# Kernel optimization log

Measured on AMD Instinct MI355X. Metric: run time of the kernel, lower is better.

The kernel has to match this reference:

```python
import jax, jax.numpy as jnp
import numpy as np

H = 32          # phasor harmonics
DELTA0 = 7.0    # base phasor frequency
HID = 128       # hidden_dim
NEXP = 4        # num_experts
EDIM = 64       # expert_dim
NCLS = 3        # num_classes
IN_DIM = 28 * 28
ENH_DIM = HID + 2 * H  # 192


def setup_inputs() -> dict:
    key = jax.random.key(0)
    ks = jax.random.split(key, 12)
    B = 65536
    s = lambda d: 1.0 / np.sqrt(d)
    return {
        "x": jax.random.normal(ks[0], (B, 28, 28), dtype=jnp.float32),
        "W_in": jax.random.normal(ks[1], (IN_DIM, HID), dtype=jnp.float32) * s(IN_DIM),
        "b_in": jnp.zeros((HID,), dtype=jnp.float32),
        "W_gate": jax.random.normal(ks[2], (ENH_DIM, NEXP), dtype=jnp.float32) * s(ENH_DIM),
        "b_gate": jnp.zeros((NEXP,), dtype=jnp.float32),
        "W_exp": jax.random.normal(ks[3], (NEXP, ENH_DIM, EDIM), dtype=jnp.float32) * s(ENH_DIM),
        "b_exp": jnp.zeros((NEXP, EDIM), dtype=jnp.float32),
        "W_ctx": jax.random.normal(ks[4], (EDIM, HID), dtype=jnp.float32) * s(EDIM),
        "b_ctx": jnp.zeros((HID,), dtype=jnp.float32),
        "W_out": jax.random.normal(ks[5], (HID, NCLS), dtype=jnp.float32) * s(HID),
        "b_out": jnp.zeros((NCLS,), dtype=jnp.float32),
    }


def _phasor_bank(t):
    # t: [B] scalar drive per sample -> [B, 2H] cos/sin harmonic features
    freqs = DELTA0 * jnp.arange(1, H + 1, dtype=t.dtype)  # [H]
    phase = t[:, None] * freqs[None, :]                   # [B, H]
    return jnp.concatenate([jnp.cos(phase), jnp.sin(phase)], axis=-1)


def reference(x, W_in, b_in, W_gate, b_gate, W_exp, b_exp, W_ctx, b_ctx, W_out, b_out):
    B = x.shape[0]
    x_flat = x.reshape((B, -1))                                  # [B, 784]
    projected = x_flat @ W_in + b_in                             # [B, HID]
    t = jnp.mean(projected, axis=-1)                             # [B]
    temporal = _phasor_bank(t)                                   # [B, 2H]
    enhanced = jnp.concatenate([projected, temporal], axis=-1)   # [B, ENH_DIM]
    # Expert retrieval core: softmax gate over NEXP experts
    gate = jax.nn.softmax(enhanced @ W_gate + b_gate, axis=-1)   # [B, NEXP]
    expert_out = jax.nn.relu(
        jnp.einsum('bd,edh->beh', enhanced, W_exp) + b_exp[None] # [B, NEXP, EDIM]
    )
    combined = jnp.einsum('be,beh->bh', gate, expert_out)        # [B, EDIM]
    context = jnp.tanh(combined @ W_ctx + b_ctx)                 # [B, HID]
    logits = context @ W_out + b_out                             # [B, NCLS]
    return logits
```

## Files before the change

### kernel.cpp

```cpp
#include <hip/hip_runtime.h>

typedef unsigned short u16;
typedef unsigned int u32;
typedef __attribute__((ext_vector_type(8))) short short8;
typedef __attribute__((ext_vector_type(4))) float f32x4;

#define OFF_WM    0
#define OFF_WINF  3584
#define OFF_WEGF  208384
#define OFF_WCTXF 312832
#define OFF_WOUTF 329216

__device__ __forceinline__ u16 f2bf(float x) {
  union { float f; u32 u; } v; v.f = x;
  u32 r = v.u + 0x7FFFu + ((v.u >> 16) & 1u);
  return (u16)(r >> 16);
}

__global__ void prep_kernel(const float* __restrict__ W_in, const float* __restrict__ b_in,
                            const float* __restrict__ W_gate, const float* __restrict__ W_exp,
                            const float* __restrict__ W_ctx, const float* __restrict__ W_out,
                            float* __restrict__ wm, u16* __restrict__ WinF,
                            u16* __restrict__ WegF, u16* __restrict__ WctxF,
                            u16* __restrict__ WoutF) {
  int idx = blockIdx.x * 256 + threadIdx.x;
  if (idx < 801) {
    if (idx == 800) {
      float s = 0.f;
      for (int j = 0; j < 128; ++j) s += b_in[j];
      wm[800] = s * (1.f / 128.f);
    } else if (idx >= 784) {
      wm[idx] = 0.f;
    } else {
      float s = 0.f;
      for (int j = 0; j < 128; ++j) s += W_in[idx * 128 + j];
      wm[idx] = s * (1.f / 128.f);
    }
  } else if (idx < 103201) {
    int f = idx - 801;
    int j = f & 7, lane = (f >> 3) & 63, tile = f >> 9;
    int ct = tile & 7, kt = tile >> 3;
    int k = kt * 32 + ((lane >> 4) << 3) + j;
    int n = ct * 16 + (lane & 15);
    WinF[f] = (k < 784) ? f2bf(W_in[k * 128 + n]) : (u16)0;
  } else if (idx < 155425) {
    int f = idx - 103201;
    int j = f & 7, lane = (f >> 3) & 63, tile = f >> 9;
    int kt = tile / 17, ct = tile - kt * 17;
    int k = kt * 32 + ((lane >> 4) << 3) + j;
    int n = ct * 16 + (lane & 15);
    float v = 0.f;
    if (n < 256) { int e = n >> 6, h = n & 63; v = W_exp[(e * 192 + k) * 64 + h]; }
    else if (n < 260) v = W_gate[k * 4 + (n - 256)];
    WegF[f] = f2bf(v);
  } else if (idx < 163617) {
    int f = idx - 155425;
    int j = f & 7, lane = (f >> 3) & 63, tile = f >> 9;
    int ct = tile & 7, kt = tile >> 3;
    int k = kt * 32 + ((lane >> 4) << 3) + j;
    int n = ct * 16 + (lane & 15);
    WctxF[f] = f2bf(W_ctx[k * 128 + n]);
  } else if (idx < 165665) {
    int f = idx - 163617;
    int j = f & 7, lane = (f >> 3) & 63, kt = f >> 9;
    int k = kt * 32 + ((lane >> 4) << 3) + j;
    int n = lane & 15;
    WoutF[f] = (n < 3) ? f2bf(W_out[k * 3 + n]) : (u16)0;
  }
}

__global__ __launch_bounds__(256, 4)
void fused_kernel(const float* __restrict__ x,
                  const float* __restrict__ b_in, const float* __restrict__ b_gate,
                  const float* __restrict__ b_exp, const float* __restrict__ b_ctx,
                  const float* __restrict__ b_out,
                  const float* __restrict__ wm, const u16* __restrict__ WinF,
                  const u16* __restrict__ WegF, const u16* __restrict__ WctxF,
                  const u16* __restrict__ WoutF,
                  float* __restrict__ out) {
  __shared__ __align__(16) u16 smem[4 * 3840];
  const int tid = threadIdx.x;
  const int wv = tid >> 6;
  const int ln = tid & 63;
  const int cb = ln & 15;
  const int qr = ln >> 4;
  u16* enhW = smem + wv * 3840;
  u16* cmbW = enhW;
  u16* ctxW = enhW + 1280;

  const int grow = blockIdx.x * 64 + wv * 16;
  const float* xr = x + (size_t)(grow + cb) * 784;

  const f32x4 vz = {0.f, 0.f, 0.f, 0.f};

  f32x4 acc[8];
  #pragma unroll
  for (int i = 0; i < 8; ++i) acc[i] = vz;
  float tp = 0.f;

  for (int kt = 0; kt < 25; ++kt) {
    const int k0 = kt * 32 + qr * 8;
    float4 a0 = make_float4(0.f, 0.f, 0.f, 0.f);
    float4 a1 = make_float4(0.f, 0.f, 0.f, 0.f);
    if (k0 < 784) {
      a0 = *(const float4*)(xr + k0);
      a1 = *(const float4*)(xr + k0 + 4);
      const float4 m0 = *(const float4*)(wm + k0);
      const float4 m1 = *(const float4*)(wm + k0 + 4);
      tp += a0.x * m0.x + a0.y * m0.y + a0.z * m0.z + a0.w * m0.w
          + a1.x * m1.x + a1.y * m1.y + a1.z * m1.z + a1.w * m1.w;
    }
    union { short8 s; u32 u[4]; } af;
    af.u[0] = (u32)f2bf(a0.x) | ((u32)f2bf(a0.y) << 16);
    af.u[1] = (u32)f2bf(a0.z) | ((u32)f2bf(a0.w) << 16);
    af.u[2] = (u32)f2bf(a1.x) | ((u32)f2bf(a1.y) << 16);
    af.u[3] = (u32)f2bf(a1.z) | ((u32)f2bf(a1.w) << 16);
    const u16* wb = WinF + (size_t)kt * 8 * 512 + ln * 8;
    #pragma unroll
    for (int ct = 0; ct < 8; ++ct) {
      short8 Bf = *(const short8*)(wb + ct * 512);
      acc[ct] = __builtin_amdgcn_mfma_f32_16x16x32_bf16(af.s, Bf, acc[ct], 0, 0, 0);
    }
  }

  tp += __shfl_xor(tp, 16);
  tp += __shfl_xor(tp, 32);
  const float t = tp + wm[800];

  #pragma unroll
  for (int ct = 0; ct < 8; ++ct) {
    float bi = b_in[ct * 16 + cb];
    u16* dst = enhW + (ct >> 1) * 640 + (ct & 1) * 16 + cb;
    #pragma unroll
    for (int i = 0; i < 4; ++i)
      dst[(qr * 4 + i) * 40] = f2bf(acc[ct][i] + bi);
  }
  {
    float phi = 7.f * t;
    float ss, cc, sd, cd;
    sincosf(phi * (float)(qr * 8 + 1), &ss, &cc);
    sincosf(phi, &sd, &cd);
    u16* pc = enhW + 4 * 640 + cb * 40 + qr * 8;
    u16* ps = enhW + 5 * 640 + cb * 40 + qr * 8;
    #pragma unroll
    for (int m = 0; m < 8; ++m) {
      pc[m] = f2bf(cc);
      ps[m] = f2bf(ss);
      float nc = cc * cd - ss * sd;
      ss = ss * cd + cc * sd;
      cc = nc;
    }
  }

  f32x4 accg = vz;
  #pragma unroll
  for (int kt = 0; kt < 6; ++kt) {
    short8 Af = *(const short8*)(enhW + kt * 640 + cb * 40 + qr * 8);
    short8 Bf = *(const short8*)(WegF + ((kt * 17 + 16) * 64 + ln) * 8);
    accg = __builtin_amdgcn_mfma_f32_16x16x32_bf16(Af, Bf, accg, 0, 0, 0);
  }
  float ge[4][4];
  {
    float bg = b_gate[cb & 3];
    #pragma unroll
    for (int i = 0; i < 4; ++i) {
      float gi = accg[i] + bg;
      float mx = fmaxf(gi, __shfl_xor(gi, 1));
      mx = fmaxf(mx, __shfl_xor(mx, 2));
      float ev = __expf(gi - mx);
      float sv = ev + __shfl_xor(ev, 1);
      sv += __shfl_xor(sv, 2);
      float g = ev / sv;
      int base = qr * 16;
      ge[0][i] = __shfl(g, base + 0);
      ge[1][i] = __shfl(g, base + 1);
      ge[2][i] = __shfl(g, base + 2);
      ge[3][i] = __shfl(g, base + 3);
    }
  }
  f32x4 cmb[4];
  #pragma unroll
  for (int i = 0; i < 4; ++i) cmb[i] = vz;
  #pragma unroll
  for (int e = 0; e < 4; ++e) {
    f32x4 ae[4];
    #pragma unroll
    for (int i = 0; i < 4; ++i) ae[i] = vz;
    #pragma unroll
    for (int kt = 0; kt < 6; ++kt) {
      short8 Af = *(const short8*)(enhW + kt * 640 + cb * 40 + qr * 8);
      #pragma unroll
      for (int c2 = 0; c2 < 4; ++c2) {
        short8 Bf = *(const short8*)(WegF + ((kt * 17 + e * 4 + c2) * 64 + ln) * 8);
        ae[c2] = __builtin_amdgcn_mfma_f32_16x16x32_bf16(Af, Bf, ae[c2], 0, 0, 0);
      }
    }
    #pragma unroll
    for (int c2 = 0; c2 < 4; ++c2) {
      float be = b_exp[e * 64 + c2 * 16 + cb];
      #pragma unroll
      for (int i = 0; i < 4; ++i)
        cmb[c2][i] += ge[e][i] * fmaxf(ae[c2][i] + be, 0.f);
    }
  }
  #pragma unroll
  for (int c2 = 0; c2 < 4; ++c2) {
    u16* dst = cmbW + (c2 >> 1) * 640 + (c2 & 1) * 16 + cb;
    #pragma unroll
    for (int i = 0; i < 4; ++i)
      dst[(qr * 4 + i) * 40] = f2bf(cmb[c2][i]);
  }

  f32x4 acc3[8];
  #pragma unroll
  for (int i = 0; i < 8; ++i) acc3[i] = vz;
  #pragma unroll
  for (int kt = 0; kt < 2; ++kt) {
    short8 Af = *(const short8*)(cmbW + kt * 640 + cb * 40 + qr * 8);
    #pragma unroll
    for (int ct = 0; ct < 8; ++ct) {
      short8 Bf = *(const short8*)(WctxF + ((kt * 8 + ct) * 64 + ln) * 8);
      acc3[ct] = __builtin_amdgcn_mfma_f32_16x16x32_bf16(Af, Bf, acc3[ct], 0, 0, 0);
    }
  }
  #pragma unroll
  for (int ct = 0; ct < 8; ++ct) {
    float bc = b_ctx[ct * 16 + cb];
    u16* dst = ctxW + ct * 16 + cb;
    #pragma unroll
    for (int i = 0; i < 4; ++i) {
      float v = acc3[ct][i] + bc;
      float ex = __expf(2.f * v);
      dst[(qr * 4 + i) * 136] = f2bf(1.f - 2.f / (ex + 1.f));
    }
  }

  f32x4 acc4 = vz;
  #pragma unroll
  for (int kt = 0; kt < 4; ++kt) {
    short8 Af = *(const short8*)(ctxW + cb * 136 + kt * 32 + qr * 8);
    short8 Bf = *(const short8*)(WoutF + (kt * 64 + ln) * 8);
    acc4 = __builtin_amdgcn_mfma_f32_16x16x32_bf16(Af, Bf, acc4, 0, 0, 0);
  }
  if (cb < 3) {
    float bo = b_out[cb];
    #pragma unroll
    for (int i = 0; i < 4; ++i)
      out[(size_t)(grow + qr * 4 + i) * 3 + cb] = acc4[i] + bo;
  }
}

extern "C" void kernel_launch(void* const* d_in, const int* in_sizes, int n_in,
                              void* d_out, int out_size, void* d_ws, size_t ws_size,
                              hipStream_t stream) {
  const float* x      = (const float*)d_in[0];
  const float* W_in   = (const float*)d_in[1];
  const float* b_in   = (const float*)d_in[2];
  const float* W_gate = (const float*)d_in[3];
  const float* b_gate = (const float*)d_in[4];
  const float* W_exp  = (const float*)d_in[5];
  const float* b_exp  = (const float*)d_in[6];
  const float* W_ctx  = (const float*)d_in[7];
  const float* b_ctx  = (const float*)d_in[8];
  const float* W_out  = (const float*)d_in[9];
  const float* b_out  = (const float*)d_in[10];
  float* out = (float*)d_out;

  char* ws = (char*)d_ws;
  float* wm  = (float*)(ws + OFF_WM);
  u16* WinF  = (u16*)(ws + OFF_WINF);
  u16* WegF  = (u16*)(ws + OFF_WEGF);
  u16* WctxF = (u16*)(ws + OFF_WCTXF);
  u16* WoutF = (u16*)(ws + OFF_WOUTF);

  const int B = in_sizes[0] / 784;
  prep_kernel<<<648, 256, 0, stream>>>(W_in, b_in, W_gate, W_exp, W_ctx, W_out,
                                       wm, WinF, WegF, WctxF, WoutF);
  fused_kernel<<<B / 64, 256, 0, stream>>>(x, b_in, b_gate, b_exp, b_ctx, b_out,
                                           wm, WinF, WegF, WctxF, WoutF, out);
}
```

Measured before the change: 342.8 us.

## Process two 16-row tiles per wave to reuse weight fragments

Each wave now handles 32 rows (two 16-row MFMA tiles) instead of 16, so every B-fragment weight load from global memory is shared by two MFMAs throughout all stages. The weight fragments for the input projection are preloaded per k-step before the activation loads. The grid is halved, LDS per block doubles, and launch bounds drop to 2 blocks per SM, trading occupancy and register pressure for fewer weight reads per row.

```diff
diff --git a/kernel.cpp b/kernel.cpp
--- a/kernel.cpp
+++ b/kernel.cpp
@@ -69,7 +69,7 @@
   }
 }
 
-__global__ __launch_bounds__(256, 4)
+__global__ __launch_bounds__(256, 2)
 void fused_kernel(const float* __restrict__ x,
                   const float* __restrict__ b_in, const float* __restrict__ b_gate,
                   const float* __restrict__ b_exp, const float* __restrict__ b_ctx,
@@ -78,70 +78,99 @@
                   const u16* __restrict__ WegF, const u16* __restrict__ WctxF,
                   const u16* __restrict__ WoutF,
                   float* __restrict__ out) {
-  __shared__ __align__(16) u16 smem[4 * 3840];
+  __shared__ __align__(16) u16 smem[4 * 7680];
   const int tid = threadIdx.x;
   const int wv = tid >> 6;
   const int ln = tid & 63;
   const int cb = ln & 15;
   const int qr = ln >> 4;
-  u16* enhW = smem + wv * 3840;
-  u16* cmbW = enhW;
-  u16* ctxW = enhW + 1280;
-
-  const int grow = blockIdx.x * 64 + wv * 16;
-  const float* xr = x + (size_t)(grow + cb) * 784;
+  u16* enh0 = smem + wv * 7680;
+  u16* enh1 = enh0 + 3840;
+  u16* cmb0 = enh0;
+  u16* cmb1 = enh1;
+  u16* ctx0 = enh0 + 1280;
+  u16* ctx1 = enh1 + 1280;
+
+  const int grow = blockIdx.x * 128 + wv * 32;
+  const float* xr0 = x + (size_t)(grow + cb) * 784;
+  const float* xr1 = xr0 + (size_t)16 * 784;
 
   const f32x4 vz = {0.f, 0.f, 0.f, 0.f};
 
-  f32x4 acc[8];
-  #pragma unroll
-  for (int i = 0; i < 8; ++i) acc[i] = vz;
-  float tp = 0.f;
-
+  f32x4 acc0[8], acc1[8];
+  #pragma unroll
+  for (int i = 0; i < 8; ++i) { acc0[i] = vz; acc1[i] = vz; }
+  float tp0 = 0.f, tp1 = 0.f;
+
+  const u16* wbase = WinF + ln * 8;
   for (int kt = 0; kt < 25; ++kt) {
+    const u16* wb = wbase + (size_t)kt * 4096;
+    short8 Bf[8];
+    #pragma unroll
+    for (int ct = 0; ct < 8; ++ct)
+      Bf[ct] = *(const short8*)(wb + ct * 512);
+
     const int k0 = kt * 32 + qr * 8;
-    float4 a0 = make_float4(0.f, 0.f, 0.f, 0.f);
-    float4 a1 = make_float4(0.f, 0.f, 0.f, 0.f);
+    float4 a0 = make_float4(0.f, 0.f, 0.f, 0.f), a1 = a0;
+    float4 b0 = a0, b1 = a0, m0 = a0, m1 = a0;
     if (k0 < 784) {
-      a0 = *(const float4*)(xr + k0);
-      a1 = *(const float4*)(xr + k0 + 4);
-      const float4 m0 = *(const float4*)(wm + k0);
-      const float4 m1 = *(const float4*)(wm + k0 + 4);
-      tp += a0.x * m0.x + a0.y * m0.y + a0.z * m0.z + a0.w * m0.w
-          + a1.x * m1.x + a1.y * m1.y + a1.z * m1.z + a1.w * m1.w;
-    }
-    union { short8 s; u32 u[4]; } af;
+      a0 = *(const float4*)(xr0 + k0);
+      a1 = *(const float4*)(xr0 + k0 + 4);
+      b0 = *(const float4*)(xr1 + k0);
+      b1 = *(const float4*)(xr1 + k0 + 4);
+      m0 = *(const float4*)(wm + k0);
+      m1 = *(const float4*)(wm + k0 + 4);
+      tp0 += a0.x * m0.x + a0.y * m0.y + a0.z * m0.z + a0.w * m0.w
+           + a1.x * m1.x + a1.y * m1.y + a1.z * m1.z + a1.w * m1.w;
+      tp1 += b0.x * m0.x + b0.y * m0.y + b0.z * m0.z + b0.w * m0.w
+           + b1.x * m1.x + b1.y * m1.y + b1.z * m1.z + b1.w * m1.w;
+    }
+    union { short8 s; u32 u[4]; } af, bf;
     af.u[0] = (u32)f2bf(a0.x) | ((u32)f2bf(a0.y) << 16);
     af.u[1] = (u32)f2bf(a0.z) | ((u32)f2bf(a0.w) << 16);
     af.u[2] = (u32)f2bf(a1.x) | ((u32)f2bf(a1.y) << 16);
     af.u[3] = (u32)f2bf(a1.z) | ((u32)f2bf(a1.w) << 16);
-    const u16* wb = WinF + (size_t)kt * 8 * 512 + ln * 8;
+    bf.u[0] = (u32)f2bf(b0.x) | ((u32)f2bf(b0.y) << 16);
+    bf.u[1] = (u32)f2bf(b0.z) | ((u32)f2bf(b0.w) << 16);
+    bf.u[2] = (u32)f2bf(b1.x) | ((u32)f2bf(b1.y) << 16);
+    bf.u[3] = (u32)f2bf(b1.z) | ((u32)f2bf(b1.w) << 16);
+
     #pragma unroll
     for (int ct = 0; ct < 8; ++ct) {
-      short8 Bf = *(const short8*)(wb + ct * 512);
-      acc[ct] = __builtin_amdgcn_mfma_f32_16x16x32_bf16(af.s, Bf, acc[ct], 0, 0, 0);
-    }
-  }
-
-  tp += __shfl_xor(tp, 16);
-  tp += __shfl_xor(tp, 32);
-  const float t = tp + wm[800];
+      acc0[ct] = __builtin_amdgcn_mfma_f32_16x16x32_bf16(af.s, Bf[ct], acc0[ct], 0, 0, 0);
+      acc1[ct] = __builtin_amdgcn_mfma_f32_16x16x32_bf16(bf.s, Bf[ct], acc1[ct], 0, 0, 0);
+    }
+  }
+
+  tp0 += __shfl_xor(tp0, 16);
+  tp0 += __shfl_xor(tp0, 32);
+  tp1 += __shfl_xor(tp1, 16);
+  tp1 += __shfl_xor(tp1, 32);
+  const float mb = wm[800];
+  const float t0 = tp0 + mb;
+  const float t1 = tp1 + mb;
 
   #pragma unroll
   for (int ct = 0; ct < 8; ++ct) {
     float bi = b_in[ct * 16 + cb];
-    u16* dst = enhW + (ct >> 1) * 640 + (ct & 1) * 16 + cb;
-    #pragma unroll
-    for (int i = 0; i < 4; ++i)
-      dst[(qr * 4 + i) * 40] = f2bf(acc[ct][i] + bi);
-  }
-  {
+    u16* d0 = enh0 + (ct >> 1) * 640 + (ct & 1) * 16 + cb;
+    u16* d1 = enh1 + (ct >> 1) * 640 + (ct & 1) * 16 + cb;
+    #pragma unroll
+    for (int i = 0; i < 4; ++i) {
+      d0[(qr * 4 + i) * 40] = f2bf(acc0[ct][i] + bi);
+      d1[(qr * 4 + i) * 40] = f2bf(acc1[ct][i] + bi);
+    }
+  }
+  #pragma unroll
+  for (int g = 0; g < 2; ++g) {
+    float t = g ? t1 : t0;
+    u16* eW = g ? enh1 : enh0;
     float phi = 7.f * t;
     float ss, cc, sd, cd;
     sincosf(phi * (float)(qr * 8 + 1), &ss, &cc);
     sincosf(phi, &sd, &cd);
-    u16* pc = enhW + 4 * 640 + cb * 40 + qr * 8;
-    u16* ps = enhW + 5 * 640 + cb * 40 + qr * 8;
+    u16* pc = eW + 4 * 640 + cb * 40 + qr * 8;
+    u16* ps = eW + 5 * 640 + cb * 40 + qr * 8;
     #pragma unroll
     for (int m = 0; m < 8; ++m) {
       pc[m] = f2bf(cc);
@@ -152,101 +181,140 @@
     }
   }
 
-  f32x4 accg = vz;
+  const u16* gbase = WegF + ln * 8;
+  f32x4 g0 = vz, g1 = vz;
   #pragma unroll
   for (int kt = 0; kt < 6; ++kt) {
-    short8 Af = *(const short8*)(enhW + kt * 640 + cb * 40 + qr * 8);
-    short8 Bf = *(const short8*)(WegF + ((kt * 17 + 16) * 64 + ln) * 8);
-    accg = __builtin_amdgcn_mfma_f32_16x16x32_bf16(Af, Bf, accg, 0, 0, 0);
-  }
-  float ge[4][4];
+    short8 A0 = *(const short8*)(enh0 + kt * 640 + cb * 40 + qr * 8);
+    short8 A1 = *(const short8*)(enh1 + kt * 640 + cb * 40 + qr * 8);
+    short8 Bg = *(const short8*)(gbase + (size_t)(kt * 17 + 16) * 512);
+    g0 = __builtin_amdgcn_mfma_f32_16x16x32_bf16(A0, Bg, g0, 0, 0, 0);
+    g1 = __builtin_amdgcn_mfma_f32_16x16x32_bf16(A1, Bg, g1, 0, 0, 0);
+  }
+
+  float ge0[4][4], ge1[4][4];
   {
     float bg = b_gate[cb & 3];
     #pragma unroll
     for (int i = 0; i < 4; ++i) {
-      float gi = accg[i] + bg;
-      float mx = fmaxf(gi, __shfl_xor(gi, 1));
-      mx = fmaxf(mx, __shfl_xor(mx, 2));
-      float ev = __expf(gi - mx);
-      float sv = ev + __shfl_xor(ev, 1);
-      sv += __shfl_xor(sv, 2);
-      float g = ev / sv;
-      int base = qr * 16;
-      ge[0][i] = __shfl(g, base + 0);
-      ge[1][i] = __shfl(g, base + 1);
-      ge[2][i] = __shfl(g, base + 2);
-      ge[3][i] = __shfl(g, base + 3);
-    }
-  }
-  f32x4 cmb[4];
-  #pragma unroll
-  for (int i = 0; i < 4; ++i) cmb[i] = vz;
+      {
+        float gi = g0[i] + bg;
+        float mx = fmaxf(gi, __shfl_xor(gi, 1));
+        mx = fmaxf(mx, __shfl_xor(mx, 2));
+        float ev = __expf(gi - mx);
+        float sv = ev + __shfl_xor(ev, 1);
+        sv += __shfl_xor(sv, 2);
+        float g = ev / sv;
+        int base = qr * 16;
+        ge0[0][i] = __shfl(g, base + 0);
+        ge0[1][i] = __shfl(g, base + 1);
+        ge0[2][i] = __shfl(g, base + 2);
+        ge0[3][i] = __shfl(g, base + 3);
+      }
+      {
+        float gi = g1[i] + bg;
+        float mx = fmaxf(gi, __shfl_xor(gi, 1));
+        mx = fmaxf(mx, __shfl_xor(mx, 2));
+        float ev = __expf(gi - mx);
+        float sv = ev + __shfl_xor(ev, 1);
+        sv += __shfl_xor(sv, 2);
+        float g = ev / sv;
+        int base = qr * 16;
+        ge1[0][i] = __shfl(g, base + 0);
+        ge1[1][i] = __shfl(g, base + 1);
+        ge1[2][i] = __shfl(g, base + 2);
+        ge1[3][i] = __shfl(g, base + 3);
+      }
+    }
+  }
+
+  f32x4 cA[4], cB[4];
+  #pragma unroll
+  for (int i = 0; i < 4; ++i) { cA[i] = vz; cB[i] = vz; }
   #pragma unroll
   for (int e = 0; e < 4; ++e) {
-    f32x4 ae[4];
-    #pragma unroll
-    for (int i = 0; i < 4; ++i) ae[i] = vz;
+    f32x4 ae0[4], ae1[4];
+    #pragma unroll
+    for (int i = 0; i < 4; ++i) { ae0[i] = vz; ae1[i] = vz; }
     #pragma unroll
     for (int kt = 0; kt < 6; ++kt) {
-      short8 Af = *(const short8*)(enhW + kt * 640 + cb * 40 + qr * 8);
+      short8 A0 = *(const short8*)(enh0 + kt * 640 + cb * 40 + qr * 8);
+      short8 A1 = *(const short8*)(enh1 + kt * 640 + cb * 40 + qr * 8);
+      const u16* gb = gbase + (size_t)(kt * 17 + e * 4) * 512;
       #pragma unroll
       for (int c2 = 0; c2 < 4; ++c2) {
-        short8 Bf = *(const short8*)(WegF + ((kt * 17 + e * 4 + c2) * 64 + ln) * 8);
-        ae[c2] = __builtin_amdgcn_mfma_f32_16x16x32_bf16(Af, Bf, ae[c2], 0, 0, 0);
+        short8 Bf = *(const short8*)(gb + c2 * 512);
+        ae0[c2] = __builtin_amdgcn_mfma_f32_16x16x32_bf16(A0, Bf, ae0[c2], 0, 0, 0);
+        ae1[c2] = __builtin_amdgcn_mfma_f32_16x16x32_bf16(A1, Bf, ae1[c2], 0, 0, 0);
       }
     }
     #pragma unroll
     for (int c2 = 0; c2 < 4; ++c2) {
       float be = b_exp[e * 64 + c2 * 16 + cb];
       #pragma unroll
-      for (int i = 0; i < 4; ++i)
-        cmb[c2][i] += ge[e][i] * fmaxf(ae[c2][i] + be, 0.f);
+      for (int i = 0; i < 4; ++i) {
+        cA[c2][i] += ge0[e][i] * fmaxf(ae0[c2][i] + be, 0.f);
+        cB[c2][i] += ge1[e][i] * fmaxf(ae1[c2][i] + be, 0.f);
+      }
     }
   }
   #pragma unroll
   for (int c2 = 0; c2 < 4; ++c2) {
-    u16* dst = cmbW + (c2 >> 1) * 640 + (c2 & 1) * 16 + cb;
-    #pragma unroll
-    for (int i = 0; i < 4; ++i)
-      dst[(qr * 4 + i) * 40] = f2bf(cmb[c2][i]);
-  }
-
-  f32x4 acc3[8];
-  #pragma unroll
-  for (int i = 0; i < 8; ++i) acc3[i] = vz;
+    u16* d0 = cmb0 + (c2 >> 1) * 640 + (c2 & 1) * 16 + cb;
+    u16* d1 = cmb1 + (c2 >> 1) * 640 + (c2 & 1) * 16 + cb;
+    #pragma unroll
+    for (int i = 0; i < 4; ++i) {
+      d0[(qr * 4 + i) * 40] = f2bf(cA[c2][i]);
+      d1[(qr * 4 + i) * 40] = f2bf(cB[c2][i]);
+    }
+  }
+
+  f32x4 c30[8], c31[8];
+  #pragma unroll
+  for (int i = 0; i < 8; ++i) { c30[i] = vz; c31[i] = vz; }
   #pragma unroll
   for (int kt = 0; kt < 2; ++kt) {
-    short8 Af = *(const short8*)(cmbW + kt * 640 + cb * 40 + qr * 8);
+    short8 A0 = *(const short8*)(cmb0 + kt * 640 + cb * 40 + qr * 8);
+    short8 A1 = *(const short8*)(cmb1 + kt * 640 + cb * 40 + qr * 8);
     #pragma unroll
     for (int ct = 0; ct < 8; ++ct) {
       short8 Bf = *(const short8*)(WctxF + ((kt * 8 + ct) * 64 + ln) * 8);
-      acc3[ct] = __builtin_amdgcn_mfma_f32_16x16x32_bf16(Af, Bf, acc3[ct], 0, 0, 0);
+      c30[ct] = __builtin_amdgcn_mfma_f32_16x16x32_bf16(A0, Bf, c30[ct], 0, 0, 0);
+      c31[ct] = __builtin_amdgcn_mfma_f32_16x16x32_bf16(A1, Bf, c31[ct], 0, 0, 0);
     }
   }
   #pragma unroll
   for (int ct = 0; ct < 8; ++ct) {
     float bc = b_ctx[ct * 16 + cb];
-    u16* dst = ctxW + ct * 16 + cb;
-    #pragma unroll
-    for (int i = 0; i < 4; ++i) {
-      float v = acc3[ct][i] + bc;
-      float ex = __expf(2.f * v);
-      dst[(qr * 4 + i) * 136] = f2bf(1.f - 2.f / (ex + 1.f));
-    }
-  }
-
-  f32x4 acc4 = vz;
+    u16* d0 = ctx0 + ct * 16 + cb;
+    u16* d1 = ctx1 + ct * 16 + cb;
+    #pragma unroll
+    for (int i = 0; i < 4; ++i) {
+      float v0 = c30[ct][i] + bc;
+      float e0 = __expf(2.f * v0);
+      d0[(qr * 4 + i) * 136] = f2bf(1.f - 2.f / (e0 + 1.f));
+      float v1 = c31[ct][i] + bc;
+      float e1 = __expf(2.f * v1);
+      d1[(qr * 4 + i) * 136] = f2bf(1.f - 2.f / (e1 + 1.f));
+    }
+  }
+
+  f32x4 a40 = vz, a41 = vz;
   #pragma unroll
   for (int kt = 0; kt < 4; ++kt) {
-    short8 Af = *(const short8*)(ctxW + cb * 136 + kt * 32 + qr * 8);
+    short8 A0 = *(const short8*)(ctx0 + cb * 136 + kt * 32 + qr * 8);
+    short8 A1 = *(const short8*)(ctx1 + cb * 136 + kt * 32 + qr * 8);
     short8 Bf = *(const short8*)(WoutF + (kt * 64 + ln) * 8);
-    acc4 = __builtin_amdgcn_mfma_f32_16x16x32_bf16(Af, Bf, acc4, 0, 0, 0);
+    a40 = __builtin_amdgcn_mfma_f32_16x16x32_bf16(A0, Bf, a40, 0, 0, 0);
+    a41 = __builtin_amdgcn_mfma_f32_16x16x32_bf16(A1, Bf, a41, 0, 0, 0);
   }
   if (cb < 3) {
     float bo = b_out[cb];
     #pragma unroll
-    for (int i = 0; i < 4; ++i)
-      out[(size_t)(grow + qr * 4 + i) * 3 + cb] = acc4[i] + bo;
+    for (int i = 0; i < 4; ++i) {
+      out[(size_t)(grow + qr * 4 + i) * 3 + cb] = a40[i] + bo;
+      out[(size_t)(grow + 16 + qr * 4 + i) * 3 + cb] = a41[i] + bo;
+    }
   }
 }
 
@@ -276,6 +344,6 @@
   const int B = in_sizes[0] / 784;
   prep_kernel<<<648, 256, 0, stream>>>(W_in, b_in, W_gate, W_exp, W_ctx, W_out,
                                        wm, WinF, WegF, WctxF, WoutF);
-  fused_kernel<<<B / 64, 256, 0, stream>>>(x, b_in, b_gate, b_exp, b_ctx, b_out,
-                                           wm, WinF, WegF, WctxF, WoutF, out);
+  fused_kernel<<<B / 128, 256, 0, stream>>>(x, b_in, b_gate, b_exp, b_ctx, b_out,
+                                            wm, WinF, WegF, WctxF, WoutF, out);
 }
```

Result: no change. 339.5 us (-1.0%).
